# Kernel optimization log

Measured on AMD Instinct MI355X. Metric: run time of the kernel, lower is better.

## Reference

```python
import jax, jax.numpy as jnp
import numpy as np

# dims (must match init_kwargs / input_specs)
B_SZ = 1024
STOCH = 1024
ACT = 32
DETER = 4096
TOKENS = 8
TOKEN_DIM = DETER // TOKENS          # 512
EXPAND = 2
HIDDEN = EXPAND * TOKEN_DIM          # 1024
NHEADS = 8
HEADDIM = HIDDEN // NHEADS           # 128
DSTATE = 64
K = 4                                # conv kernel
LAYERS = 2
CONV_DIM = HIDDEN + 2 * DSTATE       # 1152
IN_PROJ_DIM = HIDDEN + CONV_DIM + NHEADS
EPS = 1e-4


def rmsnorm(x, w):
    return x * jax.lax.rsqrt(jnp.mean(x * x, axis=-1, keepdims=True) + EPS) * w


def silu(x):
    return x * jax.nn.sigmoid(x)


def setup_inputs() -> dict:
    key = jax.random.key(0)
    ks = jax.random.split(key, 16)

    def lin(k, shape, fan_in):
        return jax.random.normal(k, shape, jnp.float32) / np.sqrt(fan_in)

    # dt_bias init (inverse softplus of log-uniform dt in [1e-3, 1e-1])
    u = jax.random.uniform(ks[0], (LAYERS, NHEADS))
    dt = jnp.exp(u * (np.log(0.1) - np.log(0.001)) + np.log(0.001))
    dt = jnp.maximum(dt, 1e-4)
    dt_bias = dt + jnp.log(-jnp.expm1(-dt))

    return {
        "stoch": jax.random.normal(ks[1], (B_SZ, STOCH), jnp.float32),
        "deter": jax.random.normal(ks[2], (B_SZ, DETER), jnp.float32),
        "action": jax.random.normal(ks[3], (B_SZ, ACT), jnp.float32),
        "conv_state": jax.random.normal(ks[4], (LAYERS, B_SZ, CONV_DIM, K - 1), jnp.float32),
        "ssm_state": jax.random.normal(ks[5], (LAYERS, B_SZ, NHEADS, HEADDIM, DSTATE), jnp.float32),
        # input_proj: Linear(stoch+act -> token_dim) + RMSNorm + SiLU
        "in_proj_w": lin(ks[6], (TOKEN_DIM, STOCH + ACT), STOCH + ACT),
        "in_proj_b": jnp.zeros((TOKEN_DIM,), jnp.float32),
        "in_norm_w": jnp.ones((TOKEN_DIM,), jnp.float32),
        # per-block params, stacked over layers
        "blk_norm_w": jnp.ones((LAYERS, TOKEN_DIM), jnp.float32),
        "blk_in_w": lin(ks[7], (LAYERS, IN_PROJ_DIM, TOKEN_DIM), TOKEN_DIM),
        "blk_conv_w": lin(ks[8], (LAYERS, CONV_DIM, K), K),
        "blk_conv_b": jnp.zeros((LAYERS, CONV_DIM), jnp.float32),
        "blk_A_log": jnp.log(jax.random.uniform(ks[9], (LAYERS, NHEADS), minval=1.0, maxval=16.0)),
        "blk_D": jnp.ones((LAYERS, NHEADS), jnp.float32),
        "blk_dt_bias": dt_bias.astype(jnp.float32),
        "blk_post_norm_w": jnp.ones((LAYERS, HIDDEN), jnp.float32),
        "blk_out_w": lin(ks[10], (LAYERS, TOKEN_DIM, HIDDEN), HIDDEN),
        "blk_out_b": jnp.zeros((LAYERS, TOKEN_DIM), jnp.float32),
        "out_norm_w": jnp.ones((TOKEN_DIM,), jnp.float32),
    }


def reference(stoch, deter, action, conv_state, ssm_state,
              in_proj_w, in_proj_b, in_norm_w,
              blk_norm_w, blk_in_w, blk_conv_w, blk_conv_b,
              blk_A_log, blk_D, blk_dt_bias, blk_post_norm_w,
              blk_out_w, blk_out_b, out_norm_w):
    b = action.shape[0]
    # action normalization with detached denominator
    action = action / jax.lax.stop_gradient(jnp.maximum(jnp.abs(action), 1.0))
    inp = jnp.concatenate([stoch.reshape(b, -1), action], axis=-1)
    tok = silu(rmsnorm(inp @ in_proj_w.T + in_proj_b, in_norm_w))  # (B, token_dim)

    def block_step(x, layer):
        nw, iw, cw, cb, alog, dskip, dtb, pw, ow, ob, cs, ss = layer
        h = rmsnorm(x, nw)
        proj = h @ iw.T  # (B, hidden + conv_dim + nheads)
        z = proj[:, :HIDDEN]
        xBC = proj[:, HIDDEN:HIDDEN + CONV_DIM]
        dt_raw = proj[:, HIDDEN + CONV_DIM:]
        # depthwise causal conv on xBC with persistent state
        seq = jnp.concatenate([cs, xBC[:, :, None]], axis=-1)  # (B, conv_dim, K)
        conv = silu(jnp.einsum('ck,bck->bc', cw, seq) + cb)
        new_cs = seq[:, :, 1:]
        x_post = conv[:, :HIDDEN]
        Bp = conv[:, HIDDEN:HIDDEN + DSTATE]
        Cp = conv[:, HIDDEN + DSTATE:]
        xh = x_post.reshape(b, NHEADS, HEADDIM)
        # SSD single-step recurrence
        dt = jax.nn.softplus(dt_raw + dtb)           # (B, H)
        dA = jnp.exp(dt * (-jnp.exp(alog)))          # (B, H)
        dBx = jnp.einsum('bh,bn,bhp->bhpn', dt, Bp, xh)
        new_ss = ss * dA[:, :, None, None] + dBx     # (B, H, P, N)
        y = jnp.einsum('bhpn,bn->bhp', new_ss, Cp) + dskip[None, :, None] * xh
        gated = rmsnorm(y.reshape(b, HIDDEN) * silu(z), pw)
        out = gated @ ow.T + ob
        return x + out, (new_cs, new_ss)

    layers = (blk_norm_w, blk_in_w, blk_conv_w, blk_conv_b, blk_A_log, blk_D,
              blk_dt_bias, blk_post_norm_w, blk_out_w, blk_out_b,
              conv_state, ssm_state)
    x_final, (new_conv_state, new_ssm_state) = jax.lax.scan(block_step, tok, layers)

    x_t = rmsnorm(x_final, out_norm_w)  # (B, token_dim)
    # rolling tape of last TOKENS final-block outputs
    tape = deter.reshape(b, TOKENS, TOKEN_DIM)
    new_deter = jnp.concatenate([tape[:, 1:], x_t[:, None, :]], axis=1).reshape(b, DETER)
    return (new_deter, new_conv_state, new_ssm_state)
```

## Files before the change

### kernel.cpp

```cpp
#include <hip/hip_runtime.h>
#include <hip/hip_bf16.h>
#include <math.h>

#define B_SZ 1024
#define STOCH 1024
#define ACT 32
#define DETER 4096
#define TOKEN_DIM 512
#define HIDDEN 1024
#define NHEADS 8
#define HEADDIM 128
#define DSTATE 64
#define CONV_DIM 1152
#define IN_PROJ_DIM 2184
#define IPP2 2304
#define KIN 1088
#define EPS 0.0001f

typedef float f32x4 __attribute__((ext_vector_type(4)));
typedef __bf16 bf16x8 __attribute__((ext_vector_type(8)));
typedef __bf16 bf16x4 __attribute__((ext_vector_type(4)));

#define N0C (512 * KIN / 4)
#define N1C (2 * IPP2 * TOKEN_DIM / 4)
#define N2C (2 * TOKEN_DIM * HIDDEN / 4)
__global__ __launch_bounds__(256) void prep_weights(
    const float* __restrict__ inproj, const float* __restrict__ blkin,
    const float* __restrict__ blkout,
    __bf16* __restrict__ w0, __bf16* __restrict__ w1, __bf16* __restrict__ w2)
{
    int i = blockIdx.x * 256 + threadIdx.x;
    bf16x4 o = { (__bf16)0.f, (__bf16)0.f, (__bf16)0.f, (__bf16)0.f };
    if (i < N0C) {
        int idx = i * 4;
        int rr = idx / KIN, cc = idx % KIN;
        if (cc < STOCH + ACT) {
            float4 v = *(const float4*)(inproj + (size_t)rr * (STOCH + ACT) + cc);
            o = bf16x4{ (__bf16)v.x, (__bf16)v.y, (__bf16)v.z, (__bf16)v.w };
        }
        ((bf16x4*)w0)[i] = o;
    } else if (i < N0C + N1C) {
        int j = i - N0C;
        int idx = j * 4;
        int li  = idx / (IPP2 * TOKEN_DIM);
        int rem = idx % (IPP2 * TOKEN_DIM);
        int rr  = rem / TOKEN_DIM, cc = rem % TOKEN_DIM;
        if (rr < IN_PROJ_DIM) {
            float4 v = *(const float4*)(blkin + ((size_t)li * IN_PROJ_DIM + rr) * TOKEN_DIM + cc);
            o = bf16x4{ (__bf16)v.x, (__bf16)v.y, (__bf16)v.z, (__bf16)v.w };
        }
        ((bf16x4*)w1)[j] = o;
    } else if (i < N0C + N1C + N2C) {
        int j = i - N0C - N1C;
        float4 v = ((const float4*)blkout)[j];
        o = bf16x4{ (__bf16)v.x, (__bf16)v.y, (__bf16)v.z, (__bf16)v.w };
        ((bf16x4*)w2)[j] = o;
    }
}

__global__ __launch_bounds__(256) void prep_inp_kernel(
    const float* __restrict__ stoch, const float* __restrict__ action, __bf16* __restrict__ inp)
{
    int idx = blockIdx.x * 256 + threadIdx.x;
    if (idx >= B_SZ * KIN) return;
    int b = idx / KIN;
    int j = idx - b * KIN;
    float v = 0.f;
    if (j < STOCH) {
        v = stoch[(size_t)b * STOCH + j];
    } else if (j < STOCH + ACT) {
        float a = action[(size_t)b * ACT + (j - STOCH)];
        float m = fabsf(a);
        v = a / (m > 1.f ? m : 1.f);
    }
    inp[idx] = (__bf16)v;
}

template<bool SPLIT>
__global__ __launch_bounds__(256) void gemm_v2(
    const __bf16* __restrict__ A,
    const __bf16* __restrict__ W,
    const float* __restrict__ bias,
    float* __restrict__ C,
    int M, int N, int K, int chunk_steps)
{
    __shared__ __bf16 As[128 * 64];
    __shared__ __bf16 Ws[64 * 64];
    const int tid = threadIdx.x;
    const int bn = blockIdx.x * 64;
    const int bm = blockIdx.y * 128;
    const int nsteps = K >> 6;
    int s_begin = 0, s_end = nsteps;
    float* Cout = C;
    if (SPLIT) {
        int z = blockIdx.z;
        s_begin = z * chunk_steps;
        int se = s_begin + chunk_steps;
        s_end = se < nsteps ? se : nsteps;
        Cout = C + (size_t)z * M * N;
    }

    const int wid = tid >> 6;
    const int lane = tid & 63;
    const int wr = wid * 32;
    const int r = lane & 15;
    const int kb = (lane >> 4) * 16;

    const int row0 = tid >> 3;
    const int colb = (tid & 7) * 16;
    const int wof = row0 * 128 + (colb ^ ((row0 & 7) << 4));
    char* Asb = (char*)As;
    char* Wsb = (char*)Ws;

    const __bf16* gA = A + (size_t)(bm + row0) * K + (s_begin << 6) + (colb >> 1);
    const __bf16* gW = W + (size_t)(bn + row0) * K + (s_begin << 6) + (colb >> 1);
    const size_t aK32 = (size_t)32 * K;

    const int ar0 = wr + r;
    const int ar1 = wr + 16 + r;
    const int aswz = (ar0 & 7) << 4;
    const int bswz = (r & 7) << 4;

    f32x4 acc[2][4] = {};
    bf16x8 va0 = *(const bf16x8*)(gA);
    bf16x8 va1 = *(const bf16x8*)(gA + aK32);
    bf16x8 va2 = *(const bf16x8*)(gA + 2 * aK32);
    bf16x8 va3 = *(const bf16x8*)(gA + 3 * aK32);
    bf16x8 vw0 = *(const bf16x8*)(gW);
    bf16x8 vw1 = *(const bf16x8*)(gW + aK32);

    for (int s = s_begin; s < s_end; ++s) {
        __syncthreads();
        *(bf16x8*)(Asb + wof) = va0;
        *(bf16x8*)(Asb + wof + 32 * 128) = va1;
        *(bf16x8*)(Asb + wof + 64 * 128) = va2;
        *(bf16x8*)(Asb + wof + 96 * 128) = va3;
        *(bf16x8*)(Wsb + wof) = vw0;
        *(bf16x8*)(Wsb + wof + 32 * 128) = vw1;
        __syncthreads();
        if (s + 1 < s_end) {
            const int ko = (s + 1 - s_begin) << 6;
            va0 = *(const bf16x8*)(gA + ko);
            va1 = *(const bf16x8*)(gA + aK32 + ko);
            va2 = *(const bf16x8*)(gA + 2 * aK32 + ko);
            va3 = *(const bf16x8*)(gA + 3 * aK32 + ko);
            vw0 = *(const bf16x8*)(gW + ko);
            vw1 = *(const bf16x8*)(gW + aK32 + ko);
        }
        #pragma unroll
        for (int ks = 0; ks < 2; ++ks) {
            const int cb = ks * 64 + kb;
            bf16x8 a0 = *(const bf16x8*)(Asb + ar0 * 128 + (cb ^ aswz));
            bf16x8 a1 = *(const bf16x8*)(Asb + ar1 * 128 + (cb ^ aswz));
            bf16x8 b0 = *(const bf16x8*)(Wsb + r * 128 + (cb ^ bswz));
            bf16x8 b1 = *(const bf16x8*)(Wsb + (r + 16) * 128 + (cb ^ bswz));
            bf16x8 b2 = *(const bf16x8*)(Wsb + (r + 32) * 128 + (cb ^ bswz));
            bf16x8 b3 = *(const bf16x8*)(Wsb + (r + 48) * 128 + (cb ^ bswz));
            acc[0][0] = __builtin_amdgcn_mfma_f32_16x16x32_bf16(a0, b0, acc[0][0], 0, 0, 0);
            acc[0][1] = __builtin_amdgcn_mfma_f32_16x16x32_bf16(a0, b1, acc[0][1], 0, 0, 0);
            acc[0][2] = __builtin_amdgcn_mfma_f32_16x16x32_bf16(a0, b2, acc[0][2], 0, 0, 0);
            acc[0][3] = __builtin_amdgcn_mfma_f32_16x16x32_bf16(a0, b3, acc[0][3], 0, 0, 0);
            acc[1][0] = __builtin_amdgcn_mfma_f32_16x16x32_bf16(a1, b0, acc[1][0], 0, 0, 0);
            acc[1][1] = __builtin_amdgcn_mfma_f32_16x16x32_bf16(a1, b1, acc[1][1], 0, 0, 0);
            acc[1][2] = __builtin_amdgcn_mfma_f32_16x16x32_bf16(a1, b2, acc[1][2], 0, 0, 0);
            acc[1][3] = __builtin_amdgcn_mfma_f32_16x16x32_bf16(a1, b3, acc[1][3], 0, 0, 0);
        }
    }

    const int cr = (lane >> 4) * 4;
    const int cc = lane & 15;
    #pragma unroll
    for (int mi = 0; mi < 2; mi++) {
        #pragma unroll
        for (int ni = 0; ni < 4; ni++) {
            int n = bn + ni * 16 + cc;
            #pragma unroll
            for (int j = 0; j < 4; j++) {
                int m = bm + wr + mi * 16 + cr + j;
                float v = acc[mi][ni][j];
                if (!SPLIT && bias) v += bias[n];
                Cout[(size_t)m * N + n] = v;
            }
        }
    }
}

__device__ __forceinline__ float block_sum(float v, float* red, int t) {
    #pragma unroll
    for (int off = 32; off >= 1; off >>= 1) v += __shfl_xor(v, off);
    if ((t & 63) == 0) red[t >> 6] = v;
    __syncthreads();
    float tot = red[0] + red[1] + red[2] + red[3];
    __syncthreads();
    return tot;
}

__global__ __launch_bounds__(256) void reduce_in_kernel(
    const float* __restrict__ P,
    const float* __restrict__ bias,
    const float* __restrict__ inw,
    const float* __restrict__ nw,
    float* __restrict__ X, __bf16* __restrict__ Hb)
{
    __shared__ float red[4];
    int b = blockIdx.x, t = threadIdx.x;
    const size_t stride = (size_t)B_SZ * TOKEN_DIM;
    float h[2];
    float ss = 0.f;
    #pragma unroll
    for (int i = 0; i < 2; i++) {
        int c = t + i * 256;
        size_t o = (size_t)b * TOKEN_DIM + c;
        float v = P[o] + P[o + stride] + P[o + 2 * stride] + P[o + 3 * stride] + bias[c];
        h[i] = v;
        ss += v * v;
    }
    float tot = block_sum(ss, red, t);
    float sc = rsqrtf(tot / (float)TOKEN_DIM + EPS);
    float ss2 = 0.f;
    #pragma unroll
    for (int i = 0; i < 2; i++) {
        int c = t + i * 256;
        float v = h[i] * sc * inw[c];
        v = v / (1.f + expf(-v));
        h[i] = v;
        X[(size_t)b * TOKEN_DIM + c] = v;
        ss2 += v * v;
    }
    float tot2 = block_sum(ss2, red, t);
    float sc2 = rsqrtf(tot2 / (float)TOKEN_DIM + EPS);
    #pragma unroll
    for (int i = 0; i < 2; i++) {
        int c = t + i * 256;
        Hb[(size_t)b * TOKEN_DIM + c] = (__bf16)(h[i] * sc2 * nw[c]);
    }
}

template<int MODE>
__global__ __launch_bounds__(256) void reduce_out_kernel(
    const float* __restrict__ P,
    const float* __restrict__ ob,
    const float* __restrict__ Xin,
    const float* __restrict__ w,
    float* __restrict__ X,
    __bf16* __restrict__ Hb,
    const float* __restrict__ deter,
    float* __restrict__ out)
{
    __shared__ float red[4];
    int b = blockIdx.x, t = threadIdx.x;
    const size_t stride = (size_t)B_SZ * TOKEN_DIM;
    float h[2];
    float ss = 0.f;
    #pragma unroll
    for (int i = 0; i < 2; i++) {
        int c = t + i * 256;
        size_t o = (size_t)b * TOKEN_DIM + c;
        float v = Xin[o] + P[o] + P[o + stride] + P[o + 2 * stride] + P[o + 3 * stride] + ob[c];
        h[i] = v;
        ss += v * v;
    }
    float tot = block_sum(ss, red, t);
    float sc = rsqrtf(tot / (float)TOKEN_DIM + EPS);
    if (MODE == 0) {
        #pragma unroll
        for (int i = 0; i < 2; i++) {
            int c = t + i * 256;
            size_t o = (size_t)b * TOKEN_DIM + c;
            X[o] = h[i];
            Hb[o] = (__bf16)(h[i] * sc * w[c]);
        }
    } else {
        #pragma unroll
        for (int i = 0; i < 2; i++) {
            int c = t + i * 256;
            out[(size_t)b * DETER + 3584 + c] = h[i] * sc * w[c];
        }
        const float4* src = (const float4*)(deter + (size_t)b * DETER + TOKEN_DIM);
        float4* dst = (float4*)(out + (size_t)b * DETER);
        #pragma unroll
        for (int j = 0; j < 4; ++j) {
            int idx = t + j * 256;
            if (idx < 896) dst[idx] = src[idx];
        }
    }
}

__global__ __launch_bounds__(256) void conv_ssm_gate_kernel(
    const float* __restrict__ cs,
    const float* __restrict__ proj,
    const float* __restrict__ cw,
    const float* __restrict__ cb,
    const float* __restrict__ dtb,
    const float* __restrict__ alog,
    const float* __restrict__ Dv,
    const float* __restrict__ pw,
    const float* __restrict__ ss,
    float* __restrict__ new_cs,
    float* __restrict__ new_ss,
    __bf16* __restrict__ Gb)
{
    __shared__ float convs[CONV_DIM];
    __shared__ float yrow[HIDDEN];
    __shared__ float dts[NHEADS], dAs[NHEADS], dvs[NHEADS];
    __shared__ float red[4];

    int b = blockIdx.x, t = threadIdx.x;

    if (t < NHEADS) {
        float dtr = proj[(size_t)b * IPP2 + HIDDEN + CONV_DIM + t] + dtb[t];
        float dt = dtr > 20.f ? dtr : log1pf(expf(dtr));
        dts[t] = dt;
        dAs[t] = expf(dt * -expf(alog[t]));
        dvs[t] = Dv[t];
    }
    for (int c = t; c < CONV_DIM; c += 256) {
        const float* s = cs + ((size_t)b * CONV_DIM + c) * 3;
        float s0 = s[0], s1 = s[1], s2 = s[2];
        float xbc = proj[(size_t)b * IPP2 + HIDDEN + c];
        float4 wv = *(const float4*)(cw + c * 4);
        float v = wv.x * s0 + wv.y * s1 + wv.z * s2 + wv.w * xbc + cb[c];
        v = v / (1.f + expf(-v));
        convs[c] = v;
        float* nc = new_cs + ((size_t)b * CONV_DIM + c) * 3;
        nc[0] = s1; nc[1] = s2; nc[2] = xbc;
    }
    __syncthreads();

    const int p0 = t >> 4;
    const int nq = (t & 15) * 4;
    float4 Bv = *(const float4*)&convs[HIDDEN + nq];
    float4 Cv = *(const float4*)&convs[HIDDEN + DSTATE + nq];
    const float* basep = ss + (size_t)b * NHEADS * HEADDIM * DSTATE;
    float* baseo = new_ss + (size_t)b * NHEADS * HEADDIM * DSTATE;

    for (int h = 0; h < NHEADS; ++h) {
        float dt = dts[h], dA = dAs[h], Dk = dvs[h];
        const float* sp = basep + (size_t)h * HEADDIM * DSTATE;
        float* op = baseo + (size_t)h * HEADDIM * DSTATE;
        #pragma unroll
        for (int it = 0; it < 8; ++it) {
            int p = it * 16 + p0;
            float xp = convs[h * HEADDIM + p];
            float dtx = dt * xp;
            float4 s4 = *(const float4*)(sp + (size_t)p * DSTATE + nq);
            float4 o;
            o.x = fmaf(s4.x, dA, dtx * Bv.x);
            o.y = fmaf(s4.y, dA, dtx * Bv.y);
            o.z = fmaf(s4.z, dA, dtx * Bv.z);
            o.w = fmaf(s4.w, dA, dtx * Bv.w);
            *(float4*)(op + (size_t)p * DSTATE + nq) = o;
            float acc = o.x * Cv.x + o.y * Cv.y + o.z * Cv.z + o.w * Cv.w;
            acc += __shfl_xor(acc, 1);
            acc += __shfl_xor(acc, 2);
            acc += __shfl_xor(acc, 4);
            acc += __shfl_xor(acc, 8);
            if ((t & 15) == 0) yrow[h * HEADDIM + p] = acc + Dk * xp;
        }
    }
    __syncthreads();

    float vv[4];
    float ssum = 0.f;
    #pragma unroll
    for (int i = 0; i < 4; i++) {
        int j = t + i * 256;
        float z = proj[(size_t)b * IPP2 + j];
        float val = yrow[j] * (z / (1.f + expf(-z)));
        vv[i] = val;
        ssum += val * val;
    }
    float tot = block_sum(ssum, red, t);
    float sc = rsqrtf(tot / (float)HIDDEN + EPS);
    #pragma unroll
    for (int i = 0; i < 4; i++) {
        int j = t + i * 256;
        Gb[(size_t)b * HIDDEN + j] = (__bf16)(vv[i] * sc * pw[j]);
    }
}

extern "C" void kernel_launch(void* const* d_in, const int* in_sizes, int n_in,
                              void* d_out, int out_size, void* d_ws, size_t ws_size,
                              hipStream_t stream) {
    const float* stoch      = (const float*)d_in[0];
    const float* deter      = (const float*)d_in[1];
    const float* action     = (const float*)d_in[2];
    const float* conv_state = (const float*)d_in[3];
    const float* ssm_state  = (const float*)d_in[4];
    const float* in_proj_w  = (const float*)d_in[5];
    const float* in_proj_b  = (const float*)d_in[6];
    const float* in_norm_w  = (const float*)d_in[7];
    const float* blk_norm_w = (const float*)d_in[8];
    const float* blk_in_w   = (const float*)d_in[9];
    const float* blk_conv_w = (const float*)d_in[10];
    const float* blk_conv_b = (const float*)d_in[11];
    const float* blk_A_log  = (const float*)d_in[12];
    const float* blk_D      = (const float*)d_in[13];
    const float* blk_dt_bias= (const float*)d_in[14];
    const float* blk_post_norm_w = (const float*)d_in[15];
    const float* blk_out_w  = (const float*)d_in[16];
    const float* blk_out_b  = (const float*)d_in[17];
    const float* out_norm_w = (const float*)d_in[18];

    float* out_deter = (float*)d_out;
    float* out_cs    = out_deter + (size_t)B_SZ * DETER;
    float* out_ss    = out_cs + (size_t)2 * B_SZ * CONV_DIM * 3;

    char* ws = (char*)d_ws;
    __bf16* Wb_inproj = (__bf16*)ws;  ws += (size_t)TOKEN_DIM * KIN * 2;
    __bf16* Wb_blkin  = (__bf16*)ws;  ws += (size_t)2 * IPP2 * TOKEN_DIM * 2;
    __bf16* Wb_blkout = (__bf16*)ws;  ws += (size_t)2 * TOKEN_DIM * HIDDEN * 2;
    float*  X         = (float*)ws;   ws += (size_t)B_SZ * TOKEN_DIM * 4;
    __bf16* Hb        = (__bf16*)ws;  ws += (size_t)B_SZ * TOKEN_DIM * 2;
    float*  PROJ      = (float*)ws;   ws += (size_t)B_SZ * IPP2 * 4;
    __bf16* Gb        = (__bf16*)ws;  ws += (size_t)B_SZ * HIDDEN * 2;
    float*  PART      = (float*)ws;   ws += (size_t)4 * B_SZ * TOKEN_DIM * 4;
    __bf16* INPb = (__bf16*)PROJ;

    {
        int total = N0C + N1C + N2C;
        prep_weights<<<(total + 255) / 256, 256, 0, stream>>>(
            in_proj_w, blk_in_w, blk_out_w, Wb_inproj, Wb_blkin, Wb_blkout);
    }
    {
        int n = B_SZ * KIN;
        prep_inp_kernel<<<(n + 255) / 256, 256, 0, stream>>>(stoch, action, INPb);
    }
    {
        dim3 grid(TOKEN_DIM / 64, B_SZ / 128, 4);
        gemm_v2<true><<<grid, 256, 0, stream>>>(INPb, Wb_inproj, nullptr, PART,
                                                B_SZ, TOKEN_DIM, KIN, 5);
        reduce_in_kernel<<<B_SZ, 256, 0, stream>>>(PART, in_proj_b, in_norm_w,
                                                   blk_norm_w, X, Hb);
    }

    for (int l = 0; l < 2; ++l) {
        const __bf16* iw = Wb_blkin + (size_t)l * IPP2 * TOKEN_DIM;
        const float* cw  = blk_conv_w + (size_t)l * CONV_DIM * 4;
        const float* cbv = blk_conv_b + (size_t)l * CONV_DIM;
        const float* alog= blk_A_log + (size_t)l * NHEADS;
        const float* Dvv = blk_D + (size_t)l * NHEADS;
        const float* dtb = blk_dt_bias + (size_t)l * NHEADS;
        const float* pw  = blk_post_norm_w + (size_t)l * HIDDEN;
        const __bf16* ow = Wb_blkout + (size_t)l * TOKEN_DIM * HIDDEN;
        const float* ob  = blk_out_b + (size_t)l * TOKEN_DIM;
        const float* cs_in = conv_state + (size_t)l * B_SZ * CONV_DIM * 3;
        const float* ss_in = ssm_state + (size_t)l * B_SZ * NHEADS * HEADDIM * DSTATE;
        float* cs_out = out_cs + (size_t)l * B_SZ * CONV_DIM * 3;
        float* ss_out = out_ss + (size_t)l * B_SZ * NHEADS * HEADDIM * DSTATE;

        {
            dim3 grid(IPP2 / 64, B_SZ / 128);
            gemm_v2<false><<<grid, 256, 0, stream>>>(Hb, iw, nullptr, PROJ,
                                                     B_SZ, IPP2, TOKEN_DIM, 0);
        }
        conv_ssm_gate_kernel<<<B_SZ, 256, 0, stream>>>(
            cs_in, PROJ, cw, cbv, dtb, alog, Dvv, pw, ss_in, cs_out, ss_out, Gb);
        {
            dim3 grid(TOKEN_DIM / 64, B_SZ / 128, 4);
            gemm_v2<true><<<grid, 256, 0, stream>>>(Gb, ow, nullptr, PART,
                                                    B_SZ, TOKEN_DIM, HIDDEN, 4);
        }
        if (l == 0) {
            reduce_out_kernel<0><<<B_SZ, 256, 0, stream>>>(
                PART, ob, X, blk_norm_w + TOKEN_DIM, X, Hb, nullptr, nullptr);
        } else {
            reduce_out_kernel<1><<<B_SZ, 256, 0, stream>>>(
                PART, ob, X, out_norm_w, nullptr, nullptr, deter, out_deter);
        }
    }
}
```

Before: 308.4 us.

## Store in-projection output as bf16, merge prep kernels, restructure SSM state streaming

Three changes. The in-projection GEMM now writes its output in bf16 instead of fp32, which halves that intermediate buffer's write and read traffic at some cost in precision for z, xBC and dt. The weight-cast and input-prep kernels are merged into one launch, with the input prep vectorised to four elements per thread. The SSM state update now gives each thread four float4 chunks per row and uses nontemporal loads and stores, which shortens the shuffle reduction and keeps the large state stream from polluting the cache.

```diff
diff --git a/kernel.cpp b/kernel.cpp
--- a/kernel.cpp
+++ b/kernel.cpp
@@ -24,10 +24,13 @@
 #define N0C (512 * KIN / 4)
 #define N1C (2 * IPP2 * TOKEN_DIM / 4)
 #define N2C (2 * TOKEN_DIM * HIDDEN / 4)
-__global__ __launch_bounds__(256) void prep_weights(
+#define N3C (B_SZ * KIN / 4)
+__global__ __launch_bounds__(256) void prep_all(
     const float* __restrict__ inproj, const float* __restrict__ blkin,
     const float* __restrict__ blkout,
-    __bf16* __restrict__ w0, __bf16* __restrict__ w1, __bf16* __restrict__ w2)
+    const float* __restrict__ stoch, const float* __restrict__ action,
+    __bf16* __restrict__ w0, __bf16* __restrict__ w1, __bf16* __restrict__ w2,
+    __bf16* __restrict__ inp)
 {
     int i = blockIdx.x * 256 + threadIdx.x;
     bf16x4 o = { (__bf16)0.f, (__bf16)0.f, (__bf16)0.f, (__bf16)0.f };
@@ -55,33 +58,33 @@
         float4 v = ((const float4*)blkout)[j];
         o = bf16x4{ (__bf16)v.x, (__bf16)v.y, (__bf16)v.z, (__bf16)v.w };
         ((bf16x4*)w2)[j] = o;
-    }
-}
-
-__global__ __launch_bounds__(256) void prep_inp_kernel(
-    const float* __restrict__ stoch, const float* __restrict__ action, __bf16* __restrict__ inp)
-{
-    int idx = blockIdx.x * 256 + threadIdx.x;
-    if (idx >= B_SZ * KIN) return;
-    int b = idx / KIN;
-    int j = idx - b * KIN;
-    float v = 0.f;
-    if (j < STOCH) {
-        v = stoch[(size_t)b * STOCH + j];
-    } else if (j < STOCH + ACT) {
-        float a = action[(size_t)b * ACT + (j - STOCH)];
-        float m = fabsf(a);
-        v = a / (m > 1.f ? m : 1.f);
-    }
-    inp[idx] = (__bf16)v;
-}
-
-template<bool SPLIT>
+    } else if (i < N0C + N1C + N2C + N3C) {
+        int j = i - N0C - N1C - N2C;
+        int idx = j * 4;
+        int b = idx / KIN, c = idx % KIN;
+        if (c < STOCH) {
+            float4 v = *(const float4*)(stoch + (size_t)b * STOCH + c);
+            o = bf16x4{ (__bf16)v.x, (__bf16)v.y, (__bf16)v.z, (__bf16)v.w };
+        } else if (c < STOCH + ACT) {
+            float4 v = *(const float4*)(action + (size_t)b * ACT + (c - STOCH));
+            float4 m;
+            m.x = fabsf(v.x) > 1.f ? fabsf(v.x) : 1.f;
+            m.y = fabsf(v.y) > 1.f ? fabsf(v.y) : 1.f;
+            m.z = fabsf(v.z) > 1.f ? fabsf(v.z) : 1.f;
+            m.w = fabsf(v.w) > 1.f ? fabsf(v.w) : 1.f;
+            o = bf16x4{ (__bf16)(v.x / m.x), (__bf16)(v.y / m.y),
+                        (__bf16)(v.z / m.z), (__bf16)(v.w / m.w) };
+        }
+        ((bf16x4*)inp)[j] = o;
+    }
+}
+
+template<bool SPLIT, typename OutT>
 __global__ __launch_bounds__(256) void gemm_v2(
     const __bf16* __restrict__ A,
     const __bf16* __restrict__ W,
     const float* __restrict__ bias,
-    float* __restrict__ C,
+    OutT* __restrict__ C,
     int M, int N, int K, int chunk_steps)
 {
     __shared__ __bf16 As[128 * 64];
@@ -91,7 +94,7 @@
     const int bm = blockIdx.y * 128;
     const int nsteps = K >> 6;
     int s_begin = 0, s_end = nsteps;
-    float* Cout = C;
+    OutT* Cout = C;
     if (SPLIT) {
         int z = blockIdx.z;
         s_begin = z * chunk_steps;
@@ -179,7 +182,7 @@
                 int m = bm + wr + mi * 16 + cr + j;
                 float v = acc[mi][ni][j];
                 if (!SPLIT && bias) v += bias[n];
-                Cout[(size_t)m * N + n] = v;
+                Cout[(size_t)m * N + n] = (OutT)v;
             }
         }
     }
@@ -288,7 +291,7 @@
 
 __global__ __launch_bounds__(256) void conv_ssm_gate_kernel(
     const float* __restrict__ cs,
-    const float* __restrict__ proj,
+    const __bf16* __restrict__ proj,
     const float* __restrict__ cw,
     const float* __restrict__ cb,
     const float* __restrict__ dtb,
@@ -306,9 +309,10 @@
     __shared__ float red[4];
 
     int b = blockIdx.x, t = threadIdx.x;
+    const __bf16* prow = proj + (size_t)b * IPP2;
 
     if (t < NHEADS) {
-        float dtr = proj[(size_t)b * IPP2 + HIDDEN + CONV_DIM + t] + dtb[t];
+        float dtr = (float)prow[HIDDEN + CONV_DIM + t] + dtb[t];
         float dt = dtr > 20.f ? dtr : log1pf(expf(dtr));
         dts[t] = dt;
         dAs[t] = expf(dt * -expf(alog[t]));
@@ -317,7 +321,7 @@
     for (int c = t; c < CONV_DIM; c += 256) {
         const float* s = cs + ((size_t)b * CONV_DIM + c) * 3;
         float s0 = s[0], s1 = s[1], s2 = s[2];
-        float xbc = proj[(size_t)b * IPP2 + HIDDEN + c];
+        float xbc = (float)prow[HIDDEN + c];
         float4 wv = *(const float4*)(cw + c * 4);
         float v = wv.x * s0 + wv.y * s1 + wv.z * s2 + wv.w * xbc + cb[c];
         v = v / (1.f + expf(-v));
@@ -327,35 +331,38 @@
     }
     __syncthreads();
 
-    const int p0 = t >> 4;
-    const int nq = (t & 15) * 4;
-    float4 Bv = *(const float4*)&convs[HIDDEN + nq];
-    float4 Cv = *(const float4*)&convs[HIDDEN + DSTATE + nq];
+    const int p0 = t >> 2;
+    const int q  = t & 3;
+    f32x4 Bv[4], Cv[4];
+    #pragma unroll
+    for (int j = 0; j < 4; ++j) {
+        Bv[j] = *(const f32x4*)&convs[HIDDEN + q * 4 + j * 16];
+        Cv[j] = *(const f32x4*)&convs[HIDDEN + DSTATE + q * 4 + j * 16];
+    }
     const float* basep = ss + (size_t)b * NHEADS * HEADDIM * DSTATE;
     float* baseo = new_ss + (size_t)b * NHEADS * HEADDIM * DSTATE;
 
     for (int h = 0; h < NHEADS; ++h) {
         float dt = dts[h], dA = dAs[h], Dk = dvs[h];
-        const float* sp = basep + (size_t)h * HEADDIM * DSTATE;
-        float* op = baseo + (size_t)h * HEADDIM * DSTATE;
-        #pragma unroll
-        for (int it = 0; it < 8; ++it) {
-            int p = it * 16 + p0;
+        #pragma unroll
+        for (int it = 0; it < 2; ++it) {
+            int p = it * 64 + p0;
             float xp = convs[h * HEADDIM + p];
             float dtx = dt * xp;
-            float4 s4 = *(const float4*)(sp + (size_t)p * DSTATE + nq);
-            float4 o;
-            o.x = fmaf(s4.x, dA, dtx * Bv.x);
-            o.y = fmaf(s4.y, dA, dtx * Bv.y);
-            o.z = fmaf(s4.z, dA, dtx * Bv.z);
-            o.w = fmaf(s4.w, dA, dtx * Bv.w);
-            *(float4*)(op + (size_t)p * DSTATE + nq) = o;
-            float acc = o.x * Cv.x + o.y * Cv.y + o.z * Cv.z + o.w * Cv.w;
+            const float* sp = basep + ((size_t)h * HEADDIM + p) * DSTATE + q * 4;
+            float* op = baseo + ((size_t)h * HEADDIM + p) * DSTATE + q * 4;
+            f32x4 acc4 = {};
+            #pragma unroll
+            for (int j = 0; j < 4; ++j) {
+                f32x4 s4 = __builtin_nontemporal_load((const f32x4*)(sp + j * 16));
+                f32x4 o = s4 * dA + dtx * Bv[j];
+                __builtin_nontemporal_store(o, (f32x4*)(op + j * 16));
+                acc4 += o * Cv[j];
+            }
+            float acc = (acc4[0] + acc4[1]) + (acc4[2] + acc4[3]);
             acc += __shfl_xor(acc, 1);
             acc += __shfl_xor(acc, 2);
-            acc += __shfl_xor(acc, 4);
-            acc += __shfl_xor(acc, 8);
-            if ((t & 15) == 0) yrow[h * HEADDIM + p] = acc + Dk * xp;
+            if (q == 0) yrow[h * HEADDIM + p] = acc + Dk * xp;
         }
     }
     __syncthreads();
@@ -365,7 +372,7 @@
     #pragma unroll
     for (int i = 0; i < 4; i++) {
         int j = t + i * 256;
-        float z = proj[(size_t)b * IPP2 + j];
+        float z = (float)prow[j];
         float val = yrow[j] * (z / (1.f + expf(-z)));
         vv[i] = val;
         ssum += val * val;
@@ -412,24 +419,21 @@
     __bf16* Wb_blkout = (__bf16*)ws;  ws += (size_t)2 * TOKEN_DIM * HIDDEN * 2;
     float*  X         = (float*)ws;   ws += (size_t)B_SZ * TOKEN_DIM * 4;
     __bf16* Hb        = (__bf16*)ws;  ws += (size_t)B_SZ * TOKEN_DIM * 2;
-    float*  PROJ      = (float*)ws;   ws += (size_t)B_SZ * IPP2 * 4;
+    __bf16* PROJ      = (__bf16*)ws;  ws += (size_t)B_SZ * IPP2 * 2;
     __bf16* Gb        = (__bf16*)ws;  ws += (size_t)B_SZ * HIDDEN * 2;
     float*  PART      = (float*)ws;   ws += (size_t)4 * B_SZ * TOKEN_DIM * 4;
-    __bf16* INPb = (__bf16*)PROJ;
+    __bf16* INPb = PROJ;
 
     {
-        int total = N0C + N1C + N2C;
-        prep_weights<<<(total + 255) / 256, 256, 0, stream>>>(
-            in_proj_w, blk_in_w, blk_out_w, Wb_inproj, Wb_blkin, Wb_blkout);
-    }
-    {
-        int n = B_SZ * KIN;
-        prep_inp_kernel<<<(n + 255) / 256, 256, 0, stream>>>(stoch, action, INPb);
+        int total = N0C + N1C + N2C + N3C;
+        prep_all<<<(total + 255) / 256, 256, 0, stream>>>(
+            in_proj_w, blk_in_w, blk_out_w, stoch, action,
+            Wb_inproj, Wb_blkin, Wb_blkout, INPb);
     }
     {
         dim3 grid(TOKEN_DIM / 64, B_SZ / 128, 4);
-        gemm_v2<true><<<grid, 256, 0, stream>>>(INPb, Wb_inproj, nullptr, PART,
-                                                B_SZ, TOKEN_DIM, KIN, 5);
+        gemm_v2<true, float><<<grid, 256, 0, stream>>>(INPb, Wb_inproj, nullptr, PART,
+                                                       B_SZ, TOKEN_DIM, KIN, 5);
         reduce_in_kernel<<<B_SZ, 256, 0, stream>>>(PART, in_proj_b, in_norm_w,
                                                    blk_norm_w, X, Hb);
     }
@@ -451,15 +455,15 @@
 
         {
             dim3 grid(IPP2 / 64, B_SZ / 128);
-            gemm_v2<false><<<grid, 256, 0, stream>>>(Hb, iw, nullptr, PROJ,
-                                                     B_SZ, IPP2, TOKEN_DIM, 0);
+            gemm_v2<false, __bf16><<<grid, 256, 0, stream>>>(Hb, iw, nullptr, PROJ,
+                                                             B_SZ, IPP2, TOKEN_DIM, 0);
         }
         conv_ssm_gate_kernel<<<B_SZ, 256, 0, stream>>>(
             cs_in, PROJ, cw, cbv, dtb, alog, Dvv, pw, ss_in, cs_out, ss_out, Gb);
         {
             dim3 grid(TOKEN_DIM / 64, B_SZ / 128, 4);
-            gemm_v2<true><<<grid, 256, 0, stream>>>(Gb, ow, nullptr, PART,
-                                                    B_SZ, TOKEN_DIM, HIDDEN, 4);
+            gemm_v2<true, float><<<grid, 256, 0, stream>>>(Gb, ow, nullptr, PART,
+                                                           B_SZ, TOKEN_DIM, HIDDEN, 4);
         }
         if (l == 0) {
             reduce_out_kernel<0><<<B_SZ, 256, 0, stream>>>(
```

New measurement: 300.0 us. 2.7% less time.
